# Kernel tuning notes

Measured on AMD Instinct MI355X. Metric: run time of the kernel, lower is better.

## Reference

```python
import jax, jax.numpy as jnp
import numpy as np

V, E, H, B, T = 32000, 256, 512, 64, 24

def setup_inputs() -> dict:
    key = jax.random.key(0)
    ks = jax.random.split(key, 24)
    def n(k, shape, s=0.02):
        return jax.random.normal(k, shape, dtype=jnp.float32) * s
    inp = {
        "question_feat": n(ks[0], (B, H), 1.0),
        "image_feat": n(ks[1], (B, H), 1.0),
        "answer_seq": jax.random.randint(ks[2], (B, T), 0, V),
        "embedding": n(ks[3], (V, E)),
        "attn_W": n(ks[4], (H, 3 * H)),
        "attn_b": jnp.zeros((H,), jnp.float32),
        "v_W": n(ks[5], (1, H)),
        "fc_W": n(ks[6], (V, H)),
        "fc_b": jnp.zeros((V,), jnp.float32),
    }
    in_sizes = [E + 2 * H, H, H]  # layer0 sees cat(embed, context)=1280
    for l in range(3):
        inp[f"W_ih{l}"] = n(ks[7 + 4 * l], (4 * H, in_sizes[l]))
        inp[f"W_hh{l}"] = n(ks[8 + 4 * l], (4 * H, H))
        inp[f"b_ih{l}"] = jnp.zeros((4 * H,), jnp.float32)
        inp[f"b_hh{l}"] = jnp.zeros((4 * H,), jnp.float32)
    return inp

def _lstm_cell(x, h, c, W_ih, W_hh, b_ih, b_hh):
    # torch gate order: i, f, g, o
    g = x @ W_ih.T + b_ih + h @ W_hh.T + b_hh
    i, f, gg, o = jnp.split(g, 4, axis=-1)
    c_new = jax.nn.sigmoid(f) * c + jax.nn.sigmoid(i) * jnp.tanh(gg)
    h_new = jax.nn.sigmoid(o) * jnp.tanh(c_new)
    return h_new, c_new

def reference(question_feat, image_feat, answer_seq, embedding, attn_W, attn_b, v_W,
              fc_W, fc_b,
              W_ih0, W_hh0, b_ih0, b_hh0,
              W_ih1, W_hh1, b_ih1, b_hh1,
              W_ih2, W_hh2, b_ih2, b_hh2):
    combined = jnp.concatenate([question_feat, image_feat], axis=1)  # [B, 2H]
    x = embedding[answer_seq]            # [B, T, E]
    xs = jnp.swapaxes(x, 0, 1)           # [T, B, E]
    Ws = ((W_ih0, W_hh0, b_ih0, b_hh0),
          (W_ih1, W_hh1, b_ih1, b_hh1),
          (W_ih2, W_hh2, b_ih2, b_hh2))

    def step(carry, x_t):
        h, c, prev_attn = carry          # h, c: [3, B, H]; prev_attn: [B, H]
        energy = jnp.tanh(jnp.concatenate([prev_attn, combined], axis=1) @ attn_W.T + attn_b)
        aw = jax.nn.softmax(energy @ v_W.T, axis=1)  # [B, 1] (softmax over singleton, faithful to source)
        ctx = aw * combined                          # [B, 2H]
        cur = jnp.concatenate([x_t, ctx], axis=1)    # [B, E+2H]
        hs, cs = [], []
        for l in range(3):
            nh, nc = _lstm_cell(cur, h[l], c[l], *Ws[l])
            hs.append(nh); cs.append(nc); cur = nh
        logits = cur @ fc_W.T + fc_b                 # [B, V]
        return (jnp.stack(hs), jnp.stack(cs), cur), logits

    hdim = question_feat.shape[1]
    bsz = question_feat.shape[0]
    h0 = jnp.zeros((3, bsz, hdim), question_feat.dtype)
    c0 = jnp.zeros((3, bsz, hdim), question_feat.dtype)
    _, outs = jax.lax.scan(step, (h0, c0, question_feat), xs)
    return jnp.swapaxes(outs, 0, 1)  # [B, T, V]
```

## Files before the change

kernel.cpp:

```cpp
#include <hip/hip_runtime.h>
#include <hip/hip_bf16.h>
#include <stdint.h>


typedef short bf16x8 __attribute__((ext_vector_type(8)));
typedef float f32x4 __attribute__((ext_vector_type(4)));

#define NLSTM 96
#define NTILE_N 250
#define HSLOT 32768

__device__ __forceinline__ unsigned short f2b(float f) {
    uint32_t u = __builtin_bit_cast(uint32_t, f);
    uint32_t r = u + 0x7FFFu + ((u >> 16) & 1u);
    return (unsigned short)(r >> 16);
}
__device__ __forceinline__ float fsig(float x) {
    float e = __expf(-x);
    return __builtin_amdgcn_rcpf(1.0f + e);
}
__device__ __forceinline__ float ftanh(float x) {
    float e = __expf(-2.0f * x);
    return (1.0f - e) * __builtin_amdgcn_rcpf(1.0f + e);
}

__global__ __launch_bounds__(128) void pack_w(
    const float* __restrict__ Whh0,
    const float* __restrict__ Wih1, const float* __restrict__ Whh1,
    const float* __restrict__ Wih2, const float* __restrict__ Whh2,
    unsigned short* __restrict__ Wpk)
{
    int gid = blockIdx.x;
    int layer = gid / (32 * 64);
    int rem = gid % (32 * 64);
    int lbid = rem >> 6, r = rem & 63;
    int q = r >> 4, jj = r & 15;
    int grow = q * 512 + lbid * 16 + jj;
    int K = (layer == 0) ? 512 : 1024;
    size_t wbase = (layer == 0) ? 0
                 : (layer == 1) ? (size_t)32 * 64 * 512
                                : (size_t)32 * 64 * 512 + (size_t)32 * 64 * 1024;
    unsigned short* dst = Wpk + wbase + ((size_t)lbid * 64 + r) * K;
    const float *s0, *s1 = nullptr;
    if (layer == 0)      { s0 = Whh0 + (size_t)grow * 512; }
    else if (layer == 1) { s0 = Wih1 + (size_t)grow * 512; s1 = Whh1 + (size_t)grow * 512; }
    else                 { s0 = Wih2 + (size_t)grow * 512; s1 = Whh2 + (size_t)grow * 512; }
    {
        int k4 = threadIdx.x;
        f32x4 v = *(const f32x4*)&s0[k4 * 4];
        unsigned short o[4];
        #pragma unroll
        for (int j = 0; j < 4; ++j) o[j] = f2b(v[j]);
        *(uint64_t*)&dst[k4 * 4] = *(uint64_t*)o;
    }
    if (s1) {
        int k4 = threadIdx.x;
        f32x4 v = *(const f32x4*)&s1[k4 * 4];
        unsigned short o[4];
        #pragma unroll
        for (int j = 0; j < 4; ++j) o[j] = f2b(v[j]);
        *(uint64_t*)&dst[512 + k4 * 4] = *(uint64_t*)o;
    }
}

__global__ __launch_bounds__(256) void build_x(
    const float* __restrict__ qf,
    const float* __restrict__ imf,
    const int* __restrict__ seq,
    const float* __restrict__ emb,
    unsigned short* __restrict__ X)
{
    int r = blockIdx.x;
    int t = r >> 6, b = r & 63;
    int tok = seq[b * 24 + t];
    for (int e = threadIdx.x; e < 1280; e += 256) {
        float v;
        if (e < 256)      v = emb[(size_t)tok * 256 + e];
        else if (e < 768) v = qf[b * 512 + (e - 256)];
        else              v = imf[b * 512 + (e - 768)];
        X[(size_t)r * 1280 + e] = f2b(v);
    }
}

__global__ __launch_bounds__(256) void gemm128(
    const unsigned short* __restrict__ A, int lda,
    const float* __restrict__ Wf, int ldb,
    int K,
    const float* __restrict__ bias0,
    const float* __restrict__ bias1,
    float* __restrict__ outf, int ldo, int mblocks, int xcdq)
{
    __shared__ unsigned short lA[128 * 72];
    __shared__ unsigned short lB[128 * 72];
    int lin = blockIdx.x;
    int wg = (lin & 7) * xcdq + (lin >> 3);
    const int m0 = (wg % mblocks) * 128, n0 = (wg / mblocks) * 128;
    const int tid = threadIdx.x;
    const int lane = tid & 63, wid = tid >> 6;
    const int wm = wid >> 1, wn = wid & 1;

    f32x4 acc[4][4] = {};

    for (int kt = 0; kt < K; kt += 64) {
        #pragma unroll
        for (int c = 0; c < 4; ++c) {
            int chunk = tid + c * 256;
            int row = chunk >> 3, kc = (chunk & 7) * 8;
            *(bf16x8*)&lA[row * 72 + kc] =
                *(const bf16x8*)&A[(size_t)(m0 + row) * lda + kt + kc];
            const float* bp = &Wf[(size_t)(n0 + row) * ldb + kt + kc];
            f32x4 v0 = *(const f32x4*)bp;
            f32x4 v1 = *(const f32x4*)(bp + 4);
            unsigned short o[8];
            #pragma unroll
            for (int x = 0; x < 4; ++x) { o[x] = f2b(v0[x]); o[4 + x] = f2b(v1[x]); }
            *(bf16x8*)&lB[row * 72 + kc] = *(bf16x8*)o;
        }
        __syncthreads();
        #pragma unroll
        for (int ks = 0; ks < 64; ks += 32) {
            int kl = ks + ((lane >> 4) << 3);
            bf16x8 af[4], bfr[4];
            #pragma unroll
            for (int i = 0; i < 4; ++i)
                af[i] = *(const bf16x8*)&lA[(wm * 64 + i * 16 + (lane & 15)) * 72 + kl];
            #pragma unroll
            for (int j = 0; j < 4; ++j)
                bfr[j] = *(const bf16x8*)&lB[(wn * 64 + j * 16 + (lane & 15)) * 72 + kl];
            #pragma unroll
            for (int i = 0; i < 4; ++i)
                #pragma unroll
                for (int j = 0; j < 4; ++j)
                    acc[i][j] = __builtin_amdgcn_mfma_f32_16x16x32_bf16(
                        af[i], bfr[j], acc[i][j], 0, 0, 0);
        }
        __syncthreads();
    }

    #pragma unroll
    for (int i = 0; i < 4; ++i) {
        #pragma unroll
        for (int j = 0; j < 4; ++j) {
            int n = n0 + wn * 64 + j * 16 + (lane & 15);
            float bias = bias0[n] + bias1[n];
            #pragma unroll
            for (int r = 0; r < 4; ++r) {
                int m = m0 + wm * 64 + i * 16 + ((lane >> 4) << 2) + r;
                outf[(size_t)m * ldo + n] = acc[i][j][r] + bias;
            }
        }
    }
}

#define ISSUE_CHUNK(buf, kb0)                                                 \
    {                                                                         \
        _Pragma("unroll")                                                     \
        for (int u_ = 0; u_ < 8; ++u_) {                                      \
            int kg_ = (kb0) + u_ * 32 + lk;                                   \
            const unsigned short* hb_ = (kg_ < 512) ? A0 : A1;                \
            int kk_ = kg_ & 511;                                              \
            const unsigned short* ap_ =                                       \
                hb_ + ((kk_ >> 4) << 10) + brow16 + (kk_ & 15);               \
            asm volatile("global_load_dwordx4 %0, %1, off"                    \
                         : "=v"(buf[u_]) : "v"(ap_) : "memory");              \
        }                                                                     \
    }
#define MFMA_CHUNK(buf, kb0)                                                  \
    {                                                                         \
        _Pragma("unroll")                                                     \
        for (int u_ = 0; u_ < 8; ++u_) {                                      \
            int ksl_ = (kb0) + u_ * 32 + lk;                                  \
            _Pragma("unroll")                                                 \
            for (int q_ = 0; q_ < 4; ++q_) {                                  \
                int gx_ = ((ksl_ >> 3) ^ (lrow & 7)) << 3;                    \
                bf16x8 bq_ = *(const bf16x8*)&lb[(q_ * 16 + lrow) * K + gx_]; \
                acc[q_] = __builtin_amdgcn_mfma_f32_16x16x32_bf16(            \
                    buf[u_], bq_, acc[q_], 0, 0, 0);                          \
            }                                                                 \
        }                                                                     \
    }
#define VM_WAIT(n) { asm volatile("s_waitcnt vmcnt(" #n ")" ::: "memory");    \
                     __builtin_amdgcn_sched_barrier(0); }
#define POLL_SET(fbase)                                                       \
    {                                                                         \
        const unsigned int* fp_ = (fbase);                                    \
        while (true) {                                                        \
            unsigned ok_ =                                                    \
                (__hip_atomic_load((unsigned int*)&fp_[lane], __ATOMIC_RELAXED, \
                                   __HIP_MEMORY_SCOPE_AGENT) != 0u) &         \
                (__hip_atomic_load((unsigned int*)&fp_[64 + lane], __ATOMIC_RELAXED, \
                                   __HIP_MEMORY_SCOPE_AGENT) != 0u);          \
            if (__all(ok_)) break;                                            \
            __builtin_amdgcn_s_sleep(1);                                      \
        }                                                                     \
    }

__global__ __launch_bounds__(256, 1) void lstm_wave(
    const unsigned short* __restrict__ Wpk,
    const float* __restrict__ G0,
    const float* __restrict__ bih1, const float* __restrict__ bhh1,
    const float* __restrict__ bih2, const float* __restrict__ bhh2,
    unsigned short* __restrict__ hst,
    unsigned int* __restrict__ flags)
{
    extern __shared__ char smem[];
    unsigned short* lb = (unsigned short*)smem;
    const int bid = blockIdx.x;
    const int tid = threadIdx.x;
    const int lane = tid & 63, w = tid >> 6;
    const int lrow = lane & 15, lk = (lane >> 4) * 8;
    const int layer = bid >> 5;
    const int lbid = bid & 31;
    const int j0 = lbid * 16;

    const int K = (layer == 0) ? 512 : 1024;
    const size_t wbase = (layer == 0) ? 0
                       : (layer == 1) ? (size_t)32 * 64 * 512
                                      : (size_t)32 * 64 * 512 + (size_t)32 * 64 * 1024;
    const unsigned short* Wblk = Wpk + wbase + (size_t)lbid * 64 * K;

    {
        const int kshift = (layer == 0) ? 6 : 7;
        const int gm = (K >> 3) - 1;
        const int total = 64 << kshift;
        for (int idx = tid; idx < total; idx += 256) {
            int row = idx >> kshift, g = idx & gm;
            int gx = g ^ (row & 7);
            *(bf16x8*)&lb[row * K + gx * 8] =
                *(const bf16x8*)&Wblk[(size_t)row * K + g * 8];
        }
    }
    __syncthreads();

    unsigned short* hl = hst + (size_t)layer * 25 * HSLOT;
    const unsigned short* hlow =
        (layer > 0) ? hst + (size_t)(layer - 1) * 25 * HSLOT : nullptr;

    float pb[4] = {0.f, 0.f, 0.f, 0.f};
    if (layer == 1) {
        #pragma unroll
        for (int q = 0; q < 4; ++q)
            pb[q] = bih1[q * 512 + j0 + lrow] + bhh1[q * 512 + j0 + lrow];
    } else if (layer == 2) {
        #pragma unroll
        for (int q = 0; q < 4; ++q)
            pb[q] = bih2[q * 512 + j0 + lrow] + bhh2[q * 512 + j0 + lrow];
    }

    float creg[4] = {0.f, 0.f, 0.f, 0.f};
    const int brow16 = (w * 16 + lrow) << 4;

    for (int t = 0; t < 24; ++t) {
        float g0p[16];
        if (layer == 0) {
            const float* gp = G0 + (size_t)t * 64 * 2048;
            #pragma unroll
            for (int r = 0; r < 4; ++r) {
                int b = w * 16 + ((lane >> 4) << 2) + r;
                #pragma unroll
                for (int q = 0; q < 4; ++q)
                    g0p[r * 4 + q] = gp[(size_t)b * 2048 + q * 512 + j0 + lrow];
            }
        }

        const unsigned short* A0 = (layer == 0)
            ? hl + (size_t)t * HSLOT
            : hlow + (size_t)(t + 1) * HSLOT;
        const unsigned short* A1 = (layer == 0)
            ? A0
            : hl + (size_t)t * HSLOT;

        f32x4 acc[4] = {};
        bf16x8 bufA[8], bufB[8], bufC[8], bufD[8];

        if (layer == 0) {
            if (t > 0) POLL_SET(flags + (t - 1) * 128);
            ISSUE_CHUNK(bufA, 0); ISSUE_CHUNK(bufB, 256);
            VM_WAIT(8); MFMA_CHUNK(bufA, 0);
            VM_WAIT(0); MFMA_CHUNK(bufB, 256);
        } else {
            if (t > 0) POLL_SET(flags + (layer * 24 + t - 1) * 128);
            ISSUE_CHUNK(bufC, 512); ISSUE_CHUNK(bufD, 768);
            POLL_SET(flags + ((layer - 1) * 24 + t) * 128);
            ISSUE_CHUNK(bufA, 0); ISSUE_CHUNK(bufB, 256);
            VM_WAIT(24); MFMA_CHUNK(bufC, 512);
            VM_WAIT(16); MFMA_CHUNK(bufD, 768);
            VM_WAIT(8);  MFMA_CHUNK(bufA, 0);
            VM_WAIT(0);  MFMA_CHUNK(bufB, 256);
        }

        unsigned short* hslot = hl + (size_t)(t + 1) * HSLOT + (lbid << 10);
        #pragma unroll
        for (int r = 0; r < 4; ++r) {
            int b = w * 16 + ((lane >> 4) << 2) + r;
            float g[4];
            #pragma unroll
            for (int q = 0; q < 4; ++q) {
                float p = (layer == 0) ? g0p[r * 4 + q] : pb[q];
                g[q] = acc[q][r] + p;
            }
            float ig = fsig(g[0]);
            float fg = fsig(g[1]);
            float gg = ftanh(g[2]);
            float og = fsig(g[3]);
            float cn = fg * creg[r] + ig * gg;
            creg[r] = cn;
            float h = og * ftanh(cn);
            unsigned int hb = (unsigned int)f2b(h);
            unsigned short* hp = hslot + (b << 4) + lrow;
            asm volatile("global_store_short %0, %1, off sc1"
                         :: "v"(hp), "v"(hb) : "memory");
        }
        asm volatile("s_waitcnt vmcnt(0)" ::: "memory");
        if (lane == 0) {
            __hip_atomic_store(&flags[(layer * 24 + t) * 128 + lbid * 4 + w], 1u,
                               __ATOMIC_RELAXED, __HIP_MEMORY_SCOPE_AGENT);
        }
    }
}

#define FC_ISSUE_G(buf, ks0)                                                  \
    {                                                                         \
        _Pragma("unroll")                                                     \
        for (int u_ = 0; u_ < 4; ++u_) {                                      \
            _Pragma("unroll")                                                 \
            for (int i_ = 0; i_ < 4; ++i_) {                                  \
                int rl_ = i_ * 16 + lrow;                                     \
                int k_ = (ks0) + u_ * 32 + lk;                                \
                const unsigned short* ap_ = h2                                \
                    + (size_t)(2 * mt + wm + 1) * HSLOT                       \
                    + ((k_ >> 4) << 10) + (rl_ << 4) + (k_ & 15);             \
                asm volatile("global_load_dwordx4 %0, %1, off"                \
                             : "=v"(buf[u_ * 4 + i_]) : "v"(ap_) : "memory"); \
            }                                                                 \
        }                                                                     \
    }
#define FC_MFMA_G(buf, ks0)                                                   \
    {                                                                         \
        _Pragma("unroll")                                                     \
        for (int u_ = 0; u_ < 4; ++u_) {                                      \
            int ks_ = (ks0) + u_ * 32 + lk;                                   \
            _Pragma("unroll")                                                 \
            for (int jj_ = 0; jj_ < 4; ++jj_) {                               \
                int row_ = wn * 64 + jj_ * 16 + lrow;                         \
                int gx_ = ((ks_ >> 3) ^ (row_ & 7)) << 3;                     \
                bf16x8 bq_ = *(const bf16x8*)&lB[row_ * 512 + gx_];           \
                _Pragma("unroll")                                             \
                for (int i_ = 0; i_ < 4; ++i_)                                \
                    acc[i_][jj_] = __builtin_amdgcn_mfma_f32_16x16x32_bf16(   \
                        buf[u_ * 4 + i_], bq_, acc[i_][jj_], 0, 0, 0);        \
            }                                                                 \
        }                                                                     \
    }

__global__ __launch_bounds__(256, 1) void fc_gemm(
    const unsigned short* __restrict__ hst,
    const float* __restrict__ fcW,
    const float* __restrict__ fcb,
    float* __restrict__ out)
{
    extern __shared__ char smem[];
    unsigned short* lB = (unsigned short*)smem;
    const int tid = threadIdx.x;
    const int lane = tid & 63, w = tid >> 6;
    const int lrow = lane & 15, lk = (lane >> 4) * 8;
    const int wm = w >> 1, wn = w & 1;
    const unsigned short* h2 = hst + (size_t)2 * 25 * HSLOT;
    const int n0 = blockIdx.x * 128;

    for (int idx = tid; idx < 128 * 64; idx += 256) {
        int row = idx >> 6, g = idx & 63;
        const float* bp = &fcW[(size_t)(n0 + row) * 512 + g * 8];
        f32x4 v0 = *(const f32x4*)bp;
        f32x4 v1 = *(const f32x4*)(bp + 4);
        unsigned short o[8];
        #pragma unroll
        for (int x = 0; x < 4; ++x) { o[x] = f2b(v0[x]); o[4 + x] = f2b(v1[x]); }
        *(bf16x8*)&lB[row * 512 + ((g ^ (row & 7)) << 3)] = *(bf16x8*)o;
    }
    __syncthreads();

    for (int mt = 0; mt < 12; ++mt) {
        const int m0 = mt * 128;
        f32x4 acc[4][4] = {};

        bf16x8 gA[16], gB[16];
        FC_ISSUE_G(gA, 0); FC_ISSUE_G(gB, 128);
        VM_WAIT(16); FC_MFMA_G(gA, 0);
        FC_ISSUE_G(gA, 256);
        VM_WAIT(16); FC_MFMA_G(gB, 128);
        FC_ISSUE_G(gB, 384);
        VM_WAIT(16); FC_MFMA_G(gA, 256);
        VM_WAIT(0);  FC_MFMA_G(gB, 384);

        #pragma unroll
        for (int i = 0; i < 4; ++i) {
            #pragma unroll
            for (int jj = 0; jj < 4; ++jj) {
                int n = n0 + wn * 64 + jj * 16 + lrow;
                float bias = fcb[n];
                #pragma unroll
                for (int r = 0; r < 4; ++r) {
                    int m = m0 + wm * 64 + i * 16 + ((lane >> 4) << 2) + r;
                    int b = m & 63, t = m >> 6;
                    __builtin_nontemporal_store(
                        acc[i][jj][r] + bias,
                        &out[(size_t)(b * 24 + t) * 32000 + n]);
                }
            }
        }
    }
}

extern "C" void kernel_launch(void* const* d_in, const int* in_sizes, int n_in,
                              void* d_out, int out_size, void* d_ws, size_t ws_size,
                              hipStream_t stream) {
    const float* qf  = (const float*)d_in[0];
    const float* imf = (const float*)d_in[1];
    const int*   seq = (const int*)d_in[2];
    const float* emb = (const float*)d_in[3];
    const float* fcW = (const float*)d_in[7];
    const float* fcb = (const float*)d_in[8];
    const float* Wih[3] = {(const float*)d_in[9],  (const float*)d_in[13], (const float*)d_in[17]};
    const float* Whh[3] = {(const float*)d_in[10], (const float*)d_in[14], (const float*)d_in[18]};
    const float* bih[3] = {(const float*)d_in[11], (const float*)d_in[15], (const float*)d_in[19]};
    const float* bhh[3] = {(const float*)d_in[12], (const float*)d_in[16], (const float*)d_in[20]};

    char* ws = (char*)d_ws;
    unsigned short* X     = (unsigned short*)(ws + 0);
    float*          G0    = (float*)(ws + 3932160);
    unsigned short* hst   = (unsigned short*)(ws + 16515072);
    unsigned int*   flags = (unsigned int*)(ws + 21430272);
    unsigned short* Wpk   = (unsigned short*)(ws + 21467136);

    hipMemsetAsync(flags, 0, 36864, stream);
    for (int l = 0; l < 3; ++l)
        hipMemsetAsync(hst + (size_t)l * 25 * HSLOT, 0, HSLOT * 2, stream);

    pack_w<<<3 * 32 * 64, 128, 0, stream>>>(Whh[0], Wih[1], Whh[1], Wih[2], Whh[2], Wpk);
    build_x<<<1536, 256, 0, stream>>>(qf, imf, seq, emb, X);

    gemm128<<<192, 256, 0, stream>>>(
        X, 1280, Wih[0], 1280, 1280, bih[0], bhh[0], G0, 2048, 12, 192 / 8);

    lstm_wave<<<NLSTM, 256, 131072, stream>>>(
        Wpk, G0, bih[1], bhh[1], bih[2], bhh[2], hst, flags);

    fc_gemm<<<NTILE_N, 256, 131072, stream>>>(
        hst, fcW, fcb, (float*)d_out);
}
```

Before: 309.5 us.

## Fuse LSTM recurrence and FC projection into one persistent flag-synchronized kernel

Merges the LSTM wavefront kernel and the FC GEMM into one launch. 96 blocks run the recurrence while 160 extra blocks convert fcW tiles to bf16 in LDS and then poll per-timestep flags, so the FC for earlier timesteps overlaps the remaining LSTM steps. The flag layout changes so each wave polls only the 32 flags for its batch slice rather than all 128. This relies on all 256 blocks being co-resident (one block per CU on a 256-CU device) and adds polling traffic, and each FC block now handles up to two N tiles.

```diff
diff --git a/kernel.cpp b/kernel.cpp
--- a/kernel.cpp
+++ b/kernel.cpp
@@ -7,6 +7,7 @@
 typedef float f32x4 __attribute__((ext_vector_type(4)));
 
 #define NLSTM 96
+#define FCB   160
 #define NTILE_N 250
 #define HSLOT 32768
 
@@ -181,143 +182,18 @@
     }
 #define VM_WAIT(n) { asm volatile("s_waitcnt vmcnt(" #n ")" ::: "memory");    \
                      __builtin_amdgcn_sched_barrier(0); }
-#define POLL_SET(fbase)                                                       \
+#define POLL32(fbase)                                                         \
     {                                                                         \
         const unsigned int* fp_ = (fbase);                                    \
+        int idx_ = lane & 31;                                                 \
         while (true) {                                                        \
-            unsigned ok_ =                                                    \
-                (__hip_atomic_load((unsigned int*)&fp_[lane], __ATOMIC_RELAXED, \
-                                   __HIP_MEMORY_SCOPE_AGENT) != 0u) &         \
-                (__hip_atomic_load((unsigned int*)&fp_[64 + lane], __ATOMIC_RELAXED, \
-                                   __HIP_MEMORY_SCOPE_AGENT) != 0u);          \
-            if (__all(ok_)) break;                                            \
+            unsigned v_ = __hip_atomic_load((unsigned int*)&fp_[idx_],        \
+                                            __ATOMIC_RELAXED,                 \
+                                            __HIP_MEMORY_SCOPE_AGENT);       \
+            if (__all(v_ != 0u)) break;                                       \
             __builtin_amdgcn_s_sleep(1);                                      \
         }                                                                     \
     }
-
-__global__ __launch_bounds__(256, 1) void lstm_wave(
-    const unsigned short* __restrict__ Wpk,
-    const float* __restrict__ G0,
-    const float* __restrict__ bih1, const float* __restrict__ bhh1,
-    const float* __restrict__ bih2, const float* __restrict__ bhh2,
-    unsigned short* __restrict__ hst,
-    unsigned int* __restrict__ flags)
-{
-    extern __shared__ char smem[];
-    unsigned short* lb = (unsigned short*)smem;
-    const int bid = blockIdx.x;
-    const int tid = threadIdx.x;
-    const int lane = tid & 63, w = tid >> 6;
-    const int lrow = lane & 15, lk = (lane >> 4) * 8;
-    const int layer = bid >> 5;
-    const int lbid = bid & 31;
-    const int j0 = lbid * 16;
-
-    const int K = (layer == 0) ? 512 : 1024;
-    const size_t wbase = (layer == 0) ? 0
-                       : (layer == 1) ? (size_t)32 * 64 * 512
-                                      : (size_t)32 * 64 * 512 + (size_t)32 * 64 * 1024;
-    const unsigned short* Wblk = Wpk + wbase + (size_t)lbid * 64 * K;
-
-    {
-        const int kshift = (layer == 0) ? 6 : 7;
-        const int gm = (K >> 3) - 1;
-        const int total = 64 << kshift;
-        for (int idx = tid; idx < total; idx += 256) {
-            int row = idx >> kshift, g = idx & gm;
-            int gx = g ^ (row & 7);
-            *(bf16x8*)&lb[row * K + gx * 8] =
-                *(const bf16x8*)&Wblk[(size_t)row * K + g * 8];
-        }
-    }
-    __syncthreads();
-
-    unsigned short* hl = hst + (size_t)layer * 25 * HSLOT;
-    const unsigned short* hlow =
-        (layer > 0) ? hst + (size_t)(layer - 1) * 25 * HSLOT : nullptr;
-
-    float pb[4] = {0.f, 0.f, 0.f, 0.f};
-    if (layer == 1) {
-        #pragma unroll
-        for (int q = 0; q < 4; ++q)
-            pb[q] = bih1[q * 512 + j0 + lrow] + bhh1[q * 512 + j0 + lrow];
-    } else if (layer == 2) {
-        #pragma unroll
-        for (int q = 0; q < 4; ++q)
-            pb[q] = bih2[q * 512 + j0 + lrow] + bhh2[q * 512 + j0 + lrow];
-    }
-
-    float creg[4] = {0.f, 0.f, 0.f, 0.f};
-    const int brow16 = (w * 16 + lrow) << 4;
-
-    for (int t = 0; t < 24; ++t) {
-        float g0p[16];
-        if (layer == 0) {
-            const float* gp = G0 + (size_t)t * 64 * 2048;
-            #pragma unroll
-            for (int r = 0; r < 4; ++r) {
-                int b = w * 16 + ((lane >> 4) << 2) + r;
-                #pragma unroll
-                for (int q = 0; q < 4; ++q)
-                    g0p[r * 4 + q] = gp[(size_t)b * 2048 + q * 512 + j0 + lrow];
-            }
-        }
-
-        const unsigned short* A0 = (layer == 0)
-            ? hl + (size_t)t * HSLOT
-            : hlow + (size_t)(t + 1) * HSLOT;
-        const unsigned short* A1 = (layer == 0)
-            ? A0
-            : hl + (size_t)t * HSLOT;
-
-        f32x4 acc[4] = {};
-        bf16x8 bufA[8], bufB[8], bufC[8], bufD[8];
-
-        if (layer == 0) {
-            if (t > 0) POLL_SET(flags + (t - 1) * 128);
-            ISSUE_CHUNK(bufA, 0); ISSUE_CHUNK(bufB, 256);
-            VM_WAIT(8); MFMA_CHUNK(bufA, 0);
-            VM_WAIT(0); MFMA_CHUNK(bufB, 256);
-        } else {
-            if (t > 0) POLL_SET(flags + (layer * 24 + t - 1) * 128);
-            ISSUE_CHUNK(bufC, 512); ISSUE_CHUNK(bufD, 768);
-            POLL_SET(flags + ((layer - 1) * 24 + t) * 128);
-            ISSUE_CHUNK(bufA, 0); ISSUE_CHUNK(bufB, 256);
-            VM_WAIT(24); MFMA_CHUNK(bufC, 512);
-            VM_WAIT(16); MFMA_CHUNK(bufD, 768);
-            VM_WAIT(8);  MFMA_CHUNK(bufA, 0);
-            VM_WAIT(0);  MFMA_CHUNK(bufB, 256);
-        }
-
-        unsigned short* hslot = hl + (size_t)(t + 1) * HSLOT + (lbid << 10);
-        #pragma unroll
-        for (int r = 0; r < 4; ++r) {
-            int b = w * 16 + ((lane >> 4) << 2) + r;
-            float g[4];
-            #pragma unroll
-            for (int q = 0; q < 4; ++q) {
-                float p = (layer == 0) ? g0p[r * 4 + q] : pb[q];
-                g[q] = acc[q][r] + p;
-            }
-            float ig = fsig(g[0]);
-            float fg = fsig(g[1]);
-            float gg = ftanh(g[2]);
-            float og = fsig(g[3]);
-            float cn = fg * creg[r] + ig * gg;
-            creg[r] = cn;
-            float h = og * ftanh(cn);
-            unsigned int hb = (unsigned int)f2b(h);
-            unsigned short* hp = hslot + (b << 4) + lrow;
-            asm volatile("global_store_short %0, %1, off sc1"
-                         :: "v"(hp), "v"(hb) : "memory");
-        }
-        asm volatile("s_waitcnt vmcnt(0)" ::: "memory");
-        if (lane == 0) {
-            __hip_atomic_store(&flags[(layer * 24 + t) * 128 + lbid * 4 + w], 1u,
-                               __ATOMIC_RELAXED, __HIP_MEMORY_SCOPE_AGENT);
-        }
-    }
-}
 
 #define FC_ISSUE_G(buf, ks0)                                                  \
     {                                                                         \
@@ -353,59 +229,198 @@
         }                                                                     \
     }
 
-__global__ __launch_bounds__(256, 1) void fc_gemm(
-    const unsigned short* __restrict__ hst,
+__global__ __launch_bounds__(256, 1) void fused_wave(
+    const unsigned short* __restrict__ Wpk,
+    const float* __restrict__ G0,
+    const float* __restrict__ bih1, const float* __restrict__ bhh1,
+    const float* __restrict__ bih2, const float* __restrict__ bhh2,
+    unsigned short* __restrict__ hst,
+    unsigned int* __restrict__ flags,
     const float* __restrict__ fcW,
     const float* __restrict__ fcb,
     float* __restrict__ out)
 {
     extern __shared__ char smem[];
-    unsigned short* lB = (unsigned short*)smem;
+    const int bid = blockIdx.x;
     const int tid = threadIdx.x;
     const int lane = tid & 63, w = tid >> 6;
     const int lrow = lane & 15, lk = (lane >> 4) * 8;
-    const int wm = w >> 1, wn = w & 1;
-    const unsigned short* h2 = hst + (size_t)2 * 25 * HSLOT;
-    const int n0 = blockIdx.x * 128;
-
-    for (int idx = tid; idx < 128 * 64; idx += 256) {
-        int row = idx >> 6, g = idx & 63;
-        const float* bp = &fcW[(size_t)(n0 + row) * 512 + g * 8];
-        f32x4 v0 = *(const f32x4*)bp;
-        f32x4 v1 = *(const f32x4*)(bp + 4);
-        unsigned short o[8];
-        #pragma unroll
-        for (int x = 0; x < 4; ++x) { o[x] = f2b(v0[x]); o[4 + x] = f2b(v1[x]); }
-        *(bf16x8*)&lB[row * 512 + ((g ^ (row & 7)) << 3)] = *(bf16x8*)o;
-    }
-    __syncthreads();
-
-    for (int mt = 0; mt < 12; ++mt) {
-        const int m0 = mt * 128;
-        f32x4 acc[4][4] = {};
-
-        bf16x8 gA[16], gB[16];
-        FC_ISSUE_G(gA, 0); FC_ISSUE_G(gB, 128);
-        VM_WAIT(16); FC_MFMA_G(gA, 0);
-        FC_ISSUE_G(gA, 256);
-        VM_WAIT(16); FC_MFMA_G(gB, 128);
-        FC_ISSUE_G(gB, 384);
-        VM_WAIT(16); FC_MFMA_G(gA, 256);
-        VM_WAIT(0);  FC_MFMA_G(gB, 384);
-
-        #pragma unroll
-        for (int i = 0; i < 4; ++i) {
-            #pragma unroll
-            for (int jj = 0; jj < 4; ++jj) {
-                int n = n0 + wn * 64 + jj * 16 + lrow;
-                float bias = fcb[n];
+
+    if (bid < NLSTM) {
+        unsigned short* lb = (unsigned short*)smem;
+        const int layer = bid >> 5;
+        const int lbid = bid & 31;
+        const int j0 = lbid * 16;
+
+        const int K = (layer == 0) ? 512 : 1024;
+        const size_t wbase = (layer == 0) ? 0
+                           : (layer == 1) ? (size_t)32 * 64 * 512
+                                          : (size_t)32 * 64 * 512 + (size_t)32 * 64 * 1024;
+        const unsigned short* Wblk = Wpk + wbase + (size_t)lbid * 64 * K;
+
+        {
+            const int kshift = (layer == 0) ? 6 : 7;
+            const int gm = (K >> 3) - 1;
+            const int total = 64 << kshift;
+            for (int idx = tid; idx < total; idx += 256) {
+                int row = idx >> kshift, g = idx & gm;
+                int gx = g ^ (row & 7);
+                *(bf16x8*)&lb[row * K + gx * 8] =
+                    *(const bf16x8*)&Wblk[(size_t)row * K + g * 8];
+            }
+        }
+        __syncthreads();
+
+        unsigned short* hl = hst + (size_t)layer * 25 * HSLOT;
+        const unsigned short* hlow =
+            (layer > 0) ? hst + (size_t)(layer - 1) * 25 * HSLOT : nullptr;
+
+        float pb[4] = {0.f, 0.f, 0.f, 0.f};
+        if (layer == 1) {
+            #pragma unroll
+            for (int q = 0; q < 4; ++q)
+                pb[q] = bih1[q * 512 + j0 + lrow] + bhh1[q * 512 + j0 + lrow];
+        } else if (layer == 2) {
+            #pragma unroll
+            for (int q = 0; q < 4; ++q)
+                pb[q] = bih2[q * 512 + j0 + lrow] + bhh2[q * 512 + j0 + lrow];
+        }
+
+        float creg[4] = {0.f, 0.f, 0.f, 0.f};
+        const int brow16 = (w * 16 + lrow) << 4;
+
+        for (int t = 0; t < 24; ++t) {
+            float g0p[16];
+            if (layer == 0) {
+                const float* gp = G0 + (size_t)t * 64 * 2048;
                 #pragma unroll
                 for (int r = 0; r < 4; ++r) {
-                    int m = m0 + wm * 64 + i * 16 + ((lane >> 4) << 2) + r;
-                    int b = m & 63, t = m >> 6;
-                    __builtin_nontemporal_store(
-                        acc[i][jj][r] + bias,
-                        &out[(size_t)(b * 24 + t) * 32000 + n]);
+                    int b = w * 16 + ((lane >> 4) << 2) + r;
+                    #pragma unroll
+                    for (int q = 0; q < 4; ++q)
+                        g0p[r * 4 + q] = gp[(size_t)b * 2048 + q * 512 + j0 + lrow];
+                }
+            }
+
+            const unsigned short* A0 = (layer == 0)
+                ? hl + (size_t)t * HSLOT
+                : hlow + (size_t)(t + 1) * HSLOT;
+            const unsigned short* A1 = (layer == 0)
+                ? A0
+                : hl + (size_t)t * HSLOT;
+
+            f32x4 acc[4] = {};
+            bf16x8 bufA[8], bufB[8], bufC[8], bufD[8];
+
+            if (layer == 0) {
+                if (t > 0) POLL32(flags + (t - 1) * 128 + w * 32);
+                ISSUE_CHUNK(bufA, 0); ISSUE_CHUNK(bufB, 256);
+                VM_WAIT(8); MFMA_CHUNK(bufA, 0);
+                VM_WAIT(0); MFMA_CHUNK(bufB, 256);
+            } else {
+                if (t > 0) POLL32(flags + (layer * 24 + t - 1) * 128 + w * 32);
+                ISSUE_CHUNK(bufC, 512); ISSUE_CHUNK(bufD, 768);
+                POLL32(flags + ((layer - 1) * 24 + t) * 128 + w * 32);
+                ISSUE_CHUNK(bufA, 0); ISSUE_CHUNK(bufB, 256);
+                VM_WAIT(24); MFMA_CHUNK(bufC, 512);
+                VM_WAIT(16); MFMA_CHUNK(bufD, 768);
+                VM_WAIT(8);  MFMA_CHUNK(bufA, 0);
+                VM_WAIT(0);  MFMA_CHUNK(bufB, 256);
+            }
+
+            unsigned short* hslot = hl + (size_t)(t + 1) * HSLOT + (lbid << 10);
+            #pragma unroll
+            for (int r = 0; r < 4; ++r) {
+                int b = w * 16 + ((lane >> 4) << 2) + r;
+                float g[4];
+                #pragma unroll
+                for (int q = 0; q < 4; ++q) {
+                    float p = (layer == 0) ? g0p[r * 4 + q] : pb[q];
+                    g[q] = acc[q][r] + p;
+                }
+                float ig = fsig(g[0]);
+                float fg = fsig(g[1]);
+                float gg = ftanh(g[2]);
+                float og = fsig(g[3]);
+                float cn = fg * creg[r] + ig * gg;
+                creg[r] = cn;
+                float h = og * ftanh(cn);
+                unsigned int hb = (unsigned int)f2b(h);
+                unsigned short* hp = hslot + (b << 4) + lrow;
+                asm volatile("global_store_short %0, %1, off sc1"
+                             :: "v"(hp), "v"(hb) : "memory");
+            }
+            asm volatile("s_waitcnt vmcnt(0)" ::: "memory");
+            if (lane == 0) {
+                __hip_atomic_store(&flags[(layer * 24 + t) * 128 + w * 32 + lbid], 1u,
+                                   __ATOMIC_RELAXED, __HIP_MEMORY_SCOPE_AGENT);
+            }
+        }
+    } else {
+        unsigned short* lB = (unsigned short*)smem;
+        const int f = bid - NLSTM;
+        const int wm = w >> 1, wn = w & 1;
+        const unsigned short* h2 = hst + (size_t)2 * 25 * HSLOT;
+
+        for (int p = 0; p < 2; ++p) {
+            int ntp = f + p * FCB;
+            if (ntp >= NTILE_N) break;
+            int n0 = ntp * 128;
+            __syncthreads();
+            for (int idx = tid; idx < 128 * 64; idx += 256) {
+                int row = idx >> 6, g = idx & 63;
+                const float* bp = &fcW[(size_t)(n0 + row) * 512 + g * 8];
+                f32x4 v0 = *(const f32x4*)bp;
+                f32x4 v1 = *(const f32x4*)(bp + 4);
+                unsigned short o[8];
+                #pragma unroll
+                for (int x = 0; x < 4; ++x) { o[x] = f2b(v0[x]); o[4 + x] = f2b(v1[x]); }
+                *(bf16x8*)&lB[row * 512 + ((g ^ (row & 7)) << 3)] = *(bf16x8*)o;
+            }
+            __syncthreads();
+
+            for (int mt = 0; mt < 12; ++mt) {
+                if (tid < 64) {
+                    const unsigned int* fb = flags + (2 * 24 + 2 * mt) * 128;
+                    while (true) {
+                        unsigned ok = 1u;
+                        #pragma unroll
+                        for (int s = 0; s < 4; ++s)
+                            ok &= (__hip_atomic_load((unsigned int*)&fb[s * 64 + lane],
+                                                     __ATOMIC_RELAXED,
+                                                     __HIP_MEMORY_SCOPE_AGENT) != 0u);
+                        if (__all(ok)) break;
+                        __builtin_amdgcn_s_sleep(16);
+                    }
+                }
+                __syncthreads();
+
+                f32x4 acc[4][4] = {};
+                bf16x8 gA[16], gB[16];
+                FC_ISSUE_G(gA, 0); FC_ISSUE_G(gB, 128);
+                VM_WAIT(16); FC_MFMA_G(gA, 0);
+                FC_ISSUE_G(gA, 256);
+                VM_WAIT(16); FC_MFMA_G(gB, 128);
+                FC_ISSUE_G(gB, 384);
+                VM_WAIT(16); FC_MFMA_G(gA, 256);
+                VM_WAIT(0);  FC_MFMA_G(gB, 384);
+
+                const int m0 = mt * 128;
+                #pragma unroll
+                for (int i = 0; i < 4; ++i) {
+                    #pragma unroll
+                    for (int jj = 0; jj < 4; ++jj) {
+                        int n = n0 + wn * 64 + jj * 16 + lrow;
+                        float bias = fcb[n];
+                        #pragma unroll
+                        for (int r = 0; r < 4; ++r) {
+                            int m = m0 + wm * 64 + i * 16 + ((lane >> 4) << 2) + r;
+                            int b = m & 63, t = m >> 6;
+                            __builtin_nontemporal_store(
+                                acc[i][jj][r] + bias,
+                                &out[(size_t)(b * 24 + t) * 32000 + n]);
+                        }
+                    }
                 }
             }
         }
@@ -443,9 +458,7 @@
     gemm128<<<192, 256, 0, stream>>>(
         X, 1280, Wih[0], 1280, 1280, bih[0], bhh[0], G0, 2048, 12, 192 / 8);
 
-    lstm_wave<<<NLSTM, 256, 131072, stream>>>(
-        Wpk, G0, bih[1], bhh[1], bih[2], bhh[2], hst, flags);
-
-    fc_gemm<<<NTILE_N, 256, 131072, stream>>>(
-        hst, fcW, fcb, (float*)d_out);
-}
+    fused_wave<<<NLSTM + FCB, 256, 131072, stream>>>(
+        Wpk, G0, bih[1], bhh[1], bih[2], bhh[2], hst, flags,
+        fcW, fcb, (float*)d_out);
+}
```

After: 331.2 us. +7.0%, slower.

## Fuse prep kernels and memsets, regroup LSTM flags, prefetch FC tiles

Applied to the files above, without the earlier changes.

Merges the weight packing, input building, flag zeroing and hidden-state zeroing into one prep kernel, replacing four memsets and two launches. The per-step flags are laid out so each wave polls only 32 contiguous flags written by the blocks it depends on, rather than all 128. The FC GEMM loop now issues the first two K-chunks of the next M tile before storing the current tile's results, overlapping loads with stores. This trades extra register pressure in the FC kernel for fewer launches and shorter dependency waits.

```diff
diff --git a/kernel.cpp b/kernel.cpp
--- a/kernel.cpp
+++ b/kernel.cpp
@@ -24,61 +24,64 @@
     return (1.0f - e) * __builtin_amdgcn_rcpf(1.0f + e);
 }
 
-__global__ __launch_bounds__(128) void pack_w(
+__global__ __launch_bounds__(256) void prep(
     const float* __restrict__ Whh0,
     const float* __restrict__ Wih1, const float* __restrict__ Whh1,
     const float* __restrict__ Wih2, const float* __restrict__ Whh2,
-    unsigned short* __restrict__ Wpk)
-{
-    int gid = blockIdx.x;
-    int layer = gid / (32 * 64);
-    int rem = gid % (32 * 64);
-    int lbid = rem >> 6, r = rem & 63;
-    int q = r >> 4, jj = r & 15;
-    int grow = q * 512 + lbid * 16 + jj;
-    int K = (layer == 0) ? 512 : 1024;
-    size_t wbase = (layer == 0) ? 0
-                 : (layer == 1) ? (size_t)32 * 64 * 512
-                                : (size_t)32 * 64 * 512 + (size_t)32 * 64 * 1024;
-    unsigned short* dst = Wpk + wbase + ((size_t)lbid * 64 + r) * K;
-    const float *s0, *s1 = nullptr;
-    if (layer == 0)      { s0 = Whh0 + (size_t)grow * 512; }
-    else if (layer == 1) { s0 = Wih1 + (size_t)grow * 512; s1 = Whh1 + (size_t)grow * 512; }
-    else                 { s0 = Wih2 + (size_t)grow * 512; s1 = Whh2 + (size_t)grow * 512; }
-    {
-        int k4 = threadIdx.x;
-        f32x4 v = *(const f32x4*)&s0[k4 * 4];
-        unsigned short o[4];
-        #pragma unroll
-        for (int j = 0; j < 4; ++j) o[j] = f2b(v[j]);
-        *(uint64_t*)&dst[k4 * 4] = *(uint64_t*)o;
-    }
-    if (s1) {
-        int k4 = threadIdx.x;
-        f32x4 v = *(const f32x4*)&s1[k4 * 4];
-        unsigned short o[4];
-        #pragma unroll
-        for (int j = 0; j < 4; ++j) o[j] = f2b(v[j]);
-        *(uint64_t*)&dst[512 + k4 * 4] = *(uint64_t*)o;
-    }
-}
-
-__global__ __launch_bounds__(256) void build_x(
+    unsigned short* __restrict__ Wpk,
     const float* __restrict__ qf,
     const float* __restrict__ imf,
     const int* __restrict__ seq,
     const float* __restrict__ emb,
-    unsigned short* __restrict__ X)
+    unsigned short* __restrict__ X,
+    unsigned int* __restrict__ flags,
+    unsigned short* __restrict__ hst)
 {
-    int r = blockIdx.x;
-    int t = r >> 6, b = r & 63;
-    int tok = seq[b * 24 + t];
-    for (int e = threadIdx.x; e < 1280; e += 256) {
-        float v;
-        if (e < 256)      v = emb[(size_t)tok * 256 + e];
-        else if (e < 768) v = qf[b * 512 + (e - 256)];
-        else              v = imf[b * 512 + (e - 768)];
-        X[(size_t)r * 1280 + e] = f2b(v);
+    int gid = blockIdx.x;
+    int tid = threadIdx.x;
+    if (gid < 6144) {
+        int layer = gid / (32 * 64);
+        int rem = gid % (32 * 64);
+        int lbid = rem >> 6, r = rem & 63;
+        int q = r >> 4, jj = r & 15;
+        int grow = q * 512 + lbid * 16 + jj;
+        int K = (layer == 0) ? 512 : 1024;
+        size_t wbase = (layer == 0) ? 0
+                     : (layer == 1) ? (size_t)32 * 64 * 512
+                                    : (size_t)32 * 64 * 512 + (size_t)32 * 64 * 1024;
+        unsigned short* dst = Wpk + wbase + ((size_t)lbid * 64 + r) * K;
+        const float *s0, *s1 = nullptr;
+        if (layer == 0)      { s0 = Whh0 + (size_t)grow * 512; }
+        else if (layer == 1) { s0 = Wih1 + (size_t)grow * 512; s1 = Whh1 + (size_t)grow * 512; }
+        else                 { s0 = Wih2 + (size_t)grow * 512; s1 = Whh2 + (size_t)grow * 512; }
+        int half = tid >> 7, k4 = tid & 127;
+        const float* src = (half == 0) ? s0 : s1;
+        if (src) {
+            f32x4 v = *(const f32x4*)&src[k4 * 4];
+            unsigned short o[4];
+            #pragma unroll
+            for (int j = 0; j < 4; ++j) o[j] = f2b(v[j]);
+            *(uint64_t*)&dst[half * 512 + k4 * 4] = *(uint64_t*)o;
+        }
+    } else if (gid < 7680) {
+        int r = gid - 6144;
+        int t = r >> 6, b = r & 63;
+        int tok = seq[b * 24 + t];
+        for (int e = tid; e < 1280; e += 256) {
+            float v;
+            if (e < 256)      v = emb[(size_t)tok * 256 + e];
+            else if (e < 768) v = qf[b * 512 + (e - 256)];
+            else              v = imf[b * 512 + (e - 768)];
+            X[(size_t)r * 1280 + e] = f2b(v);
+        }
+    } else {
+        int z = (gid - 7680) * 256 + tid;
+        for (int i = z; i < 9216; i += 2048) flags[i] = 0u;
+        unsigned int* h32 = (unsigned int*)hst;
+        for (int l = 0; l < 3; ++l) {
+            unsigned int* base = h32 + (size_t)l * 25 * (HSLOT / 2);
+            for (int i = z; i < HSLOT / 2; i += 2048) base[i] = 0u;
+        }
     }
 }
 
@@ -181,16 +184,15 @@
     }
 #define VM_WAIT(n) { asm volatile("s_waitcnt vmcnt(" #n ")" ::: "memory");    \
                      __builtin_amdgcn_sched_barrier(0); }
-#define POLL_SET(fbase)                                                       \
+#define POLL32(fbase)                                                         \
     {                                                                         \
         const unsigned int* fp_ = (fbase);                                    \
+        int idx_ = lane & 31;                                                 \
         while (true) {                                                        \
-            unsigned ok_ =                                                    \
-                (__hip_atomic_load((unsigned int*)&fp_[lane], __ATOMIC_RELAXED, \
-                                   __HIP_MEMORY_SCOPE_AGENT) != 0u) &         \
-                (__hip_atomic_load((unsigned int*)&fp_[64 + lane], __ATOMIC_RELAXED, \
-                                   __HIP_MEMORY_SCOPE_AGENT) != 0u);          \
-            if (__all(ok_)) break;                                            \
+            unsigned v_ = __hip_atomic_load((unsigned int*)&fp_[idx_],        \
+                                            __ATOMIC_RELAXED,                 \
+                                            __HIP_MEMORY_SCOPE_AGENT);       \
+            if (__all(v_ != 0u)) break;                                       \
             __builtin_amdgcn_s_sleep(1);                                      \
         }                                                                     \
     }
@@ -274,14 +276,14 @@
         bf16x8 bufA[8], bufB[8], bufC[8], bufD[8];
 
         if (layer == 0) {
-            if (t > 0) POLL_SET(flags + (t - 1) * 128);
+            if (t > 0) POLL32(flags + (t - 1) * 128 + w * 32);
             ISSUE_CHUNK(bufA, 0); ISSUE_CHUNK(bufB, 256);
             VM_WAIT(8); MFMA_CHUNK(bufA, 0);
             VM_WAIT(0); MFMA_CHUNK(bufB, 256);
         } else {
-            if (t > 0) POLL_SET(flags + (layer * 24 + t - 1) * 128);
+            if (t > 0) POLL32(flags + (layer * 24 + t - 1) * 128 + w * 32);
             ISSUE_CHUNK(bufC, 512); ISSUE_CHUNK(bufD, 768);
-            POLL_SET(flags + ((layer - 1) * 24 + t) * 128);
+            POLL32(flags + ((layer - 1) * 24 + t) * 128 + w * 32);
             ISSUE_CHUNK(bufA, 0); ISSUE_CHUNK(bufB, 256);
             VM_WAIT(24); MFMA_CHUNK(bufC, 512);
             VM_WAIT(16); MFMA_CHUNK(bufD, 768);
@@ -313,13 +315,13 @@
         }
         asm volatile("s_waitcnt vmcnt(0)" ::: "memory");
         if (lane == 0) {
-            __hip_atomic_store(&flags[(layer * 24 + t) * 128 + lbid * 4 + w], 1u,
+            __hip_atomic_store(&flags[(layer * 24 + t) * 128 + w * 32 + lbid], 1u,
                                __ATOMIC_RELAXED, __HIP_MEMORY_SCOPE_AGENT);
         }
     }
 }
 
-#define FC_ISSUE_G(buf, ks0)                                                  \
+#define FC_ISSUE_G(buf, mtv, ks0)                                             \
     {                                                                         \
         _Pragma("unroll")                                                     \
         for (int u_ = 0; u_ < 4; ++u_) {                                      \
@@ -328,7 +330,7 @@
                 int rl_ = i_ * 16 + lrow;                                     \
                 int k_ = (ks0) + u_ * 32 + lk;                                \
                 const unsigned short* ap_ = h2                                \
-                    + (size_t)(2 * mt + wm + 1) * HSLOT                       \
+                    + (size_t)(2 * (mtv) + wm + 1) * HSLOT                    \
                     + ((k_ >> 4) << 10) + (rl_ << 4) + (k_ & 15);             \
                 asm volatile("global_load_dwordx4 %0, %1, off"                \
                              : "=v"(buf[u_ * 4 + i_]) : "v"(ap_) : "memory"); \
@@ -349,6 +351,25 @@
                 for (int i_ = 0; i_ < 4; ++i_)                                \
                     acc[i_][jj_] = __builtin_amdgcn_mfma_f32_16x16x32_bf16(   \
                         buf[u_ * 4 + i_], bq_, acc[i_][jj_], 0, 0, 0);        \
+            }                                                                 \
+        }                                                                     \
+    }
+#define FC_STORES                                                             \
+    {                                                                         \
+        _Pragma("unroll")                                                     \
+        for (int i_ = 0; i_ < 4; ++i_) {                                      \
+            _Pragma("unroll")                                                 \
+            for (int jj_ = 0; jj_ < 4; ++jj_) {                               \
+                int n_ = n0 + wn * 64 + jj_ * 16 + lrow;                      \
+                float bias_ = fcb[n_];                                        \
+                _Pragma("unroll")                                             \
+                for (int r_ = 0; r_ < 4; ++r_) {                              \
+                    int m_ = m0 + wm * 64 + i_ * 16 + ((lane >> 4) << 2) + r_;\
+                    int b_ = m_ & 63, t_ = m_ >> 6;                           \
+                    __builtin_nontemporal_store(                              \
+                        acc[i_][jj_][r_] + bias_,                             \
+                        &out[(size_t)(b_ * 24 + t_) * 32000 + n_]);           \
+                }                                                             \
             }                                                                 \
         }                                                                     \
     }
@@ -380,35 +401,36 @@
     }
     __syncthreads();
 
-    for (int mt = 0; mt < 12; ++mt) {
+    bf16x8 gA[16], gB[16];
+
+    {
+        const int m0 = 0;
+        f32x4 acc[4][4] = {};
+        FC_ISSUE_G(gA, 0, 0); FC_ISSUE_G(gB, 0, 128);
+        VM_WAIT(16); FC_MFMA_G(gA, 0);
+        FC_ISSUE_G(gA, 0, 256);
+        VM_WAIT(16); FC_MFMA_G(gB, 128);
+        FC_ISSUE_G(gB, 0, 384);
+        VM_WAIT(16); FC_MFMA_G(gA, 256);
+        VM_WAIT(0);  FC_MFMA_G(gB, 384);
+        FC_ISSUE_G(gA, 1, 0); FC_ISSUE_G(gB, 1, 128);
+        FC_STORES;
+    }
+
+    for (int mt = 1; mt < 12; ++mt) {
         const int m0 = mt * 128;
         f32x4 acc[4][4] = {};
-
-        bf16x8 gA[16], gB[16];
-        FC_ISSUE_G(gA, 0); FC_ISSUE_G(gB, 128);
-        VM_WAIT(16); FC_MFMA_G(gA, 0);
-        FC_ISSUE_G(gA, 256);
-        VM_WAIT(16); FC_MFMA_G(gB, 128);
-        FC_ISSUE_G(gB, 384);
-        VM_WAIT(16); FC_MFMA_G(gA, 256);
-        VM_WAIT(0);  FC_MFMA_G(gB, 384);
-
-        #pragma unroll
-        for (int i = 0; i < 4; ++i) {
-            #pragma unroll
-            for (int jj = 0; jj < 4; ++jj) {
-                int n = n0 + wn * 64 + jj * 16 + lrow;
-                float bias = fcb[n];
-                #pragma unroll
-                for (int r = 0; r < 4; ++r) {
-                    int m = m0 + wm * 64 + i * 16 + ((lane >> 4) << 2) + r;
-                    int b = m & 63, t = m >> 6;
-                    __builtin_nontemporal_store(
-                        acc[i][jj][r] + bias,
-                        &out[(size_t)(b * 24 + t) * 32000 + n]);
-                }
-            }
-        }
+        VM_WAIT(63);
+        FC_MFMA_G(gA, 0);
+        FC_ISSUE_G(gA, mt, 256);
+        FC_MFMA_G(gB, 128);
+        FC_ISSUE_G(gB, mt, 384);
+        VM_WAIT(16);
+        FC_MFMA_G(gA, 256);
+        VM_WAIT(0);
+        FC_MFMA_G(gB, 384);
+        if (mt < 11) { FC_ISSUE_G(gA, mt + 1, 0); FC_ISSUE_G(gB, mt + 1, 128); }
+        FC_STORES;
     }
 }
 
@@ -433,12 +455,9 @@
     unsigned int*   flags = (unsigned int*)(ws + 21430272);
     unsigned short* Wpk   = (unsigned short*)(ws + 21467136);
 
-    hipMemsetAsync(flags, 0, 36864, stream);
-    for (int l = 0; l < 3; ++l)
-        hipMemsetAsync(hst + (size_t)l * 25 * HSLOT, 0, HSLOT * 2, stream);
-
-    pack_w<<<3 * 32 * 64, 128, 0, stream>>>(Whh[0], Wih[1], Whh[1], Wih[2], Whh[2], Wpk);
-    build_x<<<1536, 256, 0, stream>>>(qf, imf, seq, emb, X);
+    prep<<<7688, 256, 0, stream>>>(
+        Whh[0], Wih[1], Whh[1], Wih[2], Whh[2], Wpk,
+        qf, imf, seq, emb, X, flags, hst);
 
     gemm128<<<192, 256, 0, stream>>>(
         X, 1280, Wih[0], 1280, 1280, bih[0], bhh[0], G0, 2048, 12, 192 / 8);
```

After: 299.6 us. 3.2% less time.
